# Optimization experiments

Hardware: AMD Instinct MI355X
Metric: run time of the kernel (lower is better)

Reference implementation:

```python
import jax, jax.numpy as jnp
import numpy as np
from jax import lax

B, DIM, H, W = 4, 192, 128, 128
NUM_HEADS = 4
EPS = 1e-12


def _conv1x1(x, w):
    # x: [b,c,h,w], w: [o,i,1,1]
    return lax.conv_general_dilated(x, w, (1, 1), 'VALID',
                                    dimension_numbers=('NCHW', 'OIHW', 'NCHW'))


def _dwconv3x3(x, w):
    # depthwise: w: [c,1,3,3], groups = c
    return lax.conv_general_dilated(x, w, (1, 1), ((1, 1), (1, 1)),
                                    dimension_numbers=('NCHW', 'OIHW', 'NCHW'),
                                    feature_group_count=w.shape[0])


def _l2norm(t):
    # normalize along last (spatial) axis, torch F.normalize semantics
    n = jnp.sqrt(jnp.sum(t * t, axis=-1, keepdims=True))
    return t / jnp.maximum(n, EPS)


def _heads(t, b, h, w):
    # [b, head*c, h, w] -> [b, head, c, h*w]
    return t.reshape(b, NUM_HEADS, t.shape[1] // NUM_HEADS, h * w)


def setup_inputs() -> dict:
    key = jax.random.key(0)
    ks = jax.random.split(key, 9)
    s = 0.02
    return {
        'x': jax.random.normal(ks[0], (B, DIM, H, W), jnp.float32),
        'ctx': jax.random.normal(ks[1], (B, DIM, H, W), jnp.float32),
        'x_qkv_w': jax.random.normal(ks[2], (DIM * 3, DIM, 1, 1), jnp.float32) * s,
        'x_dw_w': jax.random.normal(ks[3], (DIM * 3, 1, 3, 3), jnp.float32) * s,
        'x_po_w': jax.random.normal(ks[4], (DIM, DIM, 1, 1), jnp.float32) * s,
        'ctx_qkv_w': jax.random.normal(ks[5], (DIM * 3, DIM, 1, 1), jnp.float32) * s,
        'ctx_dw_w': jax.random.normal(ks[6], (DIM * 3, 1, 3, 3), jnp.float32) * s,
        'ctx_po_w': jax.random.normal(ks[7], (DIM, DIM, 1, 1), jnp.float32) * s,
        'temperature': jnp.ones((NUM_HEADS, 1, 1), jnp.float32),
    }


def reference(x, ctx, x_qkv_w, x_dw_w, x_po_w, ctx_qkv_w, ctx_dw_w, ctx_po_w, temperature):
    b, c, h, w = x.shape
    x_qkv = _dwconv3x3(_conv1x1(x, x_qkv_w), x_dw_w)
    x_q, x_k, x_v = jnp.split(x_qkv, 3, axis=1)
    ctx_qkv = _dwconv3x3(_conv1x1(ctx, ctx_qkv_w), ctx_dw_w)
    ctx_q, ctx_k, ctx_v = jnp.split(ctx_qkv, 3, axis=1)

    x_q, x_k, x_v = (_heads(t, b, h, w) for t in (x_q, x_k, x_v))
    ctx_q, ctx_k, ctx_v = (_heads(t, b, h, w) for t in (ctx_q, ctx_k, ctx_v))

    temp = temperature[None]  # [1, head, 1, 1]

    # ctx branch: x_q attends over ctx
    q1 = _l2norm(x_q)
    k1 = _l2norm(ctx_k)
    attn1 = jax.nn.softmax(jnp.einsum('bhcn,bhdn->bhcd', q1, k1) * temp, axis=-1)
    ctx_out = jnp.einsum('bhcd,bhdn->bhcn', attn1, ctx_v).reshape(b, c, h, w)
    ctx_out = _conv1x1(ctx_out, ctx_po_w)

    # x branch: ctx_q attends over x
    q2 = _l2norm(ctx_q)
    k2 = _l2norm(x_k)
    attn2 = jax.nn.softmax(jnp.einsum('bhcn,bhdn->bhcd', q2, k2) * temp, axis=-1)
    x_out = jnp.einsum('bhcd,bhdn->bhcn', attn2, x_v).reshape(b, c, h, w)
    x_out = _conv1x1(x_out, x_po_w)

    return (x_out, ctx_out)
```

## Files before the change

### kernel.cpp

```cpp
#include <hip/hip_runtime.h>
#include <hip/hip_bf16.h>

#define N_PIX 16384
#define W_ 128

typedef __attribute__((ext_vector_type(8))) unsigned short ushort8_t;
typedef __attribute__((ext_vector_type(4))) unsigned short ushort4_t;
typedef __attribute__((ext_vector_type(8))) __bf16 bf16x8;
typedef __attribute__((ext_vector_type(4))) float f32x4;

__device__ inline float bf2f(unsigned short u) {
    return __uint_as_float(((unsigned)u) << 16);
}
__device__ inline unsigned short f2bf(float f) {
    __hip_bfloat16 h = __float2bfloat16(f);
    return *(unsigned short*)&h;
}

__global__ __launch_bounds__(256) void k_conv_mfma(
    const float* __restrict__ in,
    const float* __restrict__ w,
    unsigned short* __restrict__ out)
{
    const int p0 = blockIdx.x * 128;
    const int b  = blockIdx.y;
    const float* inb = in + (long)b * 192 * N_PIX;
    unsigned short* ob = out + (long)b * 576 * N_PIX;

    __shared__ unsigned short Xl[128 * 200];
    __shared__ unsigned short Wl[2][96 * 200];

    const int tid  = threadIdx.x;
    const int lane = tid & 63;
    const int wid  = tid >> 6;
    const int wo   = wid >> 1;
    const int wp   = wid & 1;
    const int l15  = lane & 15;
    const int lq   = lane >> 4;

    {
        const int p = tid & 127, kh = tid >> 7;
        #pragma unroll
        for (int seg = 0; seg < 12; seg++) {
            ushort8_t pk;
            #pragma unroll
            for (int j = 0; j < 8; j++)
                pk[j] = f2bf(inb[(long)(kh * 96 + seg * 8 + j) * N_PIX + p0 + p]);
            *(ushort8_t*)&Xl[p * 200 + kh * 96 + seg * 8] = pk;
        }
    }
    #pragma unroll
    for (int it = 0; it < 18; it++) {
        int idx = it * 1024 + tid * 4;
        float4 v = *(const float4*)(w + idx);
        int row = idx / 192, col = idx - row * 192;
        ushort4_t s; s[0] = f2bf(v.x); s[1] = f2bf(v.y); s[2] = f2bf(v.z); s[3] = f2bf(v.w);
        *(ushort4_t*)&Wl[0][row * 200 + col] = s;
    }

    for (int oc = 0; oc < 6; oc++) {
        __syncthreads();
        if (oc + 1 < 6) {
            const float* wc = w + (long)(oc + 1) * 96 * 192;
            #pragma unroll
            for (int it = 0; it < 18; it++) {
                int idx = it * 1024 + tid * 4;
                float4 v = *(const float4*)(wc + idx);
                int row = idx / 192, col = idx - row * 192;
                ushort4_t s; s[0] = f2bf(v.x); s[1] = f2bf(v.y); s[2] = f2bf(v.z); s[3] = f2bf(v.w);
                *(ushort4_t*)&Wl[(oc + 1) & 1][row * 200 + col] = s;
            }
        }
        const unsigned short* Wb = Wl[oc & 1];
        f32x4 acc[3][4];
        const f32x4 zero = {0.f, 0.f, 0.f, 0.f};
        #pragma unroll
        for (int i = 0; i < 3; i++)
            #pragma unroll
            for (int j = 0; j < 4; j++) acc[i][j] = zero;

        #pragma unroll
        for (int kc = 0; kc < 6; kc++) {
            bf16x8 af[3], bfv[4];
            #pragma unroll
            for (int mt = 0; mt < 3; mt++)
                af[mt] = *(const bf16x8*)&Wb[(wo * 48 + mt * 16 + l15) * 200 + kc * 32 + lq * 8];
            #pragma unroll
            for (int nt = 0; nt < 4; nt++)
                bfv[nt] = *(const bf16x8*)&Xl[(wp * 64 + nt * 16 + l15) * 200 + kc * 32 + lq * 8];
            #pragma unroll
            for (int mt = 0; mt < 3; mt++)
                #pragma unroll
                for (int nt = 0; nt < 4; nt++)
                    acc[mt][nt] = __builtin_amdgcn_mfma_f32_16x16x32_bf16(
                        af[mt], bfv[nt], acc[mt][nt], 0, 0, 0);
        }
        #pragma unroll
        for (int mt = 0; mt < 3; mt++) {
            #pragma unroll
            for (int r = 0; r < 4; r++) {
                int o = oc * 96 + wo * 48 + mt * 16 + lq * 4 + r;
                long base = (long)o * N_PIX + p0 + wp * 64 + l15;
                #pragma unroll
                for (int nt = 0; nt < 4; nt++)
                    ob[base + nt * 16] = f2bf(acc[mt][nt][r]);
            }
        }
    }
}

__global__ __launch_bounds__(256) void k_dwconv(
    const unsigned short* __restrict__ in, const float* __restrict__ w,
    unsigned short* __restrict__ out)
{
    const int m  = blockIdx.y;
    const int ch = m % 576;
    const int y0 = blockIdx.x * 16;
    const unsigned short* ip = in + (long)m * N_PIX;
    const float* wp = w + ch * 9;

    __shared__ unsigned short Ll[18][136];

    const int tid = threadIdx.x;
    #pragma unroll
    for (int idx = tid; idx < 288; idx += 256) {
        int lr = idx >> 4, lc = (idx & 15) * 8;
        int gy = y0 - 1 + lr;
        ushort8_t v;
        #pragma unroll
        for (int j = 0; j < 8; j++) v[j] = 0;
        if ((unsigned)gy <= 127u)
            v = *(const ushort8_t*)(ip + gy * W_ + lc);
        *(ushort8_t*)&Ll[lr][lc] = v;
    }
    float wv[9];
    #pragma unroll
    for (int i = 0; i < 9; i++) wv[i] = wp[i];
    __syncthreads();

    const int r  = tid >> 4;
    const int xg = (tid & 15) * 8;

    float o[8];
    #pragma unroll
    for (int j = 0; j < 8; j++) o[j] = 0.f;

    #pragma unroll
    for (int dy = 0; dy < 3; dy++) {
        const unsigned short* lrow = &Ll[r + dy][0];
        float c[10];
        c[0] = (xg == 0) ? 0.f : bf2f(lrow[xg - 1]);
        ushort8_t mid = *(const ushort8_t*)&lrow[xg];
        #pragma unroll
        for (int j = 0; j < 8; j++) c[1 + j] = bf2f(mid[j]);
        c[9] = (xg == 120) ? 0.f : bf2f(lrow[xg + 8]);
        const float w0 = wv[dy * 3], w1 = wv[dy * 3 + 1], w2 = wv[dy * 3 + 2];
        #pragma unroll
        for (int j = 0; j < 8; j++)
            o[j] = fmaf(w0, c[j], fmaf(w1, c[j + 1], fmaf(w2, c[j + 2], o[j])));
    }
    ushort8_t res;
    #pragma unroll
    for (int j = 0; j < 8; j++) res[j] = f2bf(o[j]);
    *(ushort8_t*)(out + (long)m * N_PIX + (y0 + r) * W_ + xg) = res;
}

__global__ __launch_bounds__(256) void k_gram_mfma(
    const unsigned short* __restrict__ qkv_x,
    const unsigned short* __restrict__ qkv_c,
    float* __restrict__ S, float* __restrict__ qn, float* __restrict__ kn)
{
    const int attn = blockIdx.z;
    const int bh   = blockIdx.y;
    const int b = bh >> 2, h = bh & 3;
    const unsigned short* qb =
        (attn == 0 ? qkv_x : qkv_c) + ((long)b * 576 + h * 48) * N_PIX;
    const unsigned short* kb =
        (attn == 0 ? qkv_c : qkv_x) + ((long)b * 576 + 192 + h * 48) * N_PIX;

    __shared__ float Sl[48 * 49];
    __shared__ float qnl[48], knl[48];

    const int tid = threadIdx.x;
    for (int i = tid; i < 48 * 49; i += 256) Sl[i] = 0.f;
    if (tid < 48) { qnl[tid] = 0.f; knl[tid] = 0.f; }
    __syncthreads();

    const int lane = tid & 63, wid = tid >> 6;
    const int l15 = lane & 15, lq = lane >> 4;
    const long nbase = (long)blockIdx.x * 1024 + wid * 256;

    f32x4 acc[3][3], aq[3], ak[3];
    const f32x4 zero = {0.f, 0.f, 0.f, 0.f};
    #pragma unroll
    for (int i = 0; i < 3; i++) {
        aq[i] = zero; ak[i] = zero;
        #pragma unroll
        for (int j = 0; j < 3; j++) acc[i][j] = zero;
    }

    for (int ks = 0; ks < 8; ks++) {
        const long ns = nbase + ks * 32;
        bf16x8 af[3], bfv[3];
        #pragma unroll
        for (int mt = 0; mt < 3; mt++)
            af[mt] = *(const bf16x8*)(qb + (long)(mt * 16 + l15) * N_PIX + ns + lq * 8);
        #pragma unroll
        for (int nt = 0; nt < 3; nt++)
            bfv[nt] = *(const bf16x8*)(kb + (long)(nt * 16 + l15) * N_PIX + ns + lq * 8);
        #pragma unroll
        for (int mt = 0; mt < 3; mt++)
            #pragma unroll
            for (int nt = 0; nt < 3; nt++)
                acc[mt][nt] = __builtin_amdgcn_mfma_f32_16x16x32_bf16(
                    af[mt], bfv[nt], acc[mt][nt], 0, 0, 0);
        #pragma unroll
        for (int mt = 0; mt < 3; mt++)
            aq[mt] = __builtin_amdgcn_mfma_f32_16x16x32_bf16(af[mt], af[mt], aq[mt], 0, 0, 0);
        #pragma unroll
        for (int nt = 0; nt < 3; nt++)
            ak[nt] = __builtin_amdgcn_mfma_f32_16x16x32_bf16(bfv[nt], bfv[nt], ak[nt], 0, 0, 0);
    }

    #pragma unroll
    for (int mt = 0; mt < 3; mt++)
        #pragma unroll
        for (int nt = 0; nt < 3; nt++)
            #pragma unroll
            for (int r = 0; r < 4; r++)
                atomicAdd(&Sl[(mt * 16 + lq * 4 + r) * 49 + nt * 16 + l15],
                          acc[mt][nt][r]);
    #pragma unroll
    for (int mt = 0; mt < 3; mt++)
        #pragma unroll
        for (int r = 0; r < 4; r++)
            if (l15 == lq * 4 + r) {
                atomicAdd(&qnl[mt * 16 + l15], aq[mt][r]);
                atomicAdd(&knl[mt * 16 + l15], ak[mt][r]);
            }
    __syncthreads();

    float* Sg = S + (long)(attn * 16 + bh) * 2304;
    float* qg = qn + (long)(attn * 16 + bh) * 48;
    float* kg = kn + (long)(attn * 16 + bh) * 48;
    for (int i = tid; i < 2304; i += 256) {
        int row = i / 48, col = i - row * 48;
        atomicAdd(&Sg[i], Sl[row * 49 + col]);
    }
    if (tid < 48) atomicAdd(&qg[tid], qnl[tid]);
    else if (tid < 96) atomicAdd(&kg[tid - 48], knl[tid - 48]);
}

__global__ __launch_bounds__(192) void k_softmax(
    const float* __restrict__ S, const float* __restrict__ qn,
    const float* __restrict__ kn, const float* __restrict__ temp,
    float* __restrict__ P)
{
    const int attn = blockIdx.x, b = blockIdx.y;
    const int r = threadIdx.x;
    const int h = r / 48, c = r % 48;
    const int bh = b * 4 + h;
    const float t = temp[h];
    const float* Srow = S + ((long)(attn * 16 + bh) * 48 + c) * 48;
    const float* knp  = kn + (long)(attn * 16 + bh) * 48;
    const float qc = fmaxf(sqrtf(qn[(long)(attn * 16 + bh) * 48 + c]), 1e-12f);
    float lg[48];
    float mx = -1e30f;
    #pragma unroll
    for (int d = 0; d < 48; d++) {
        float kd = fmaxf(sqrtf(knp[d]), 1e-12f);
        lg[d] = Srow[d] / (qc * kd) * t;
        mx = fmaxf(mx, lg[d]);
    }
    float sum = 0.f;
    #pragma unroll
    for (int d = 0; d < 48; d++) { lg[d] = __expf(lg[d] - mx); sum += lg[d]; }
    const float inv = 1.f / sum;
    float* Pp = P + (((long)(attn * 4 + b) * 4 + h) * 48 + c) * 48;
    #pragma unroll
    for (int d = 0; d < 48; d++) Pp[d] = lg[d] * inv;
}

__global__ __launch_bounds__(192) void k_w2(
    const float* __restrict__ P, const float* __restrict__ x_po,
    const float* __restrict__ ctx_po, unsigned short* __restrict__ W2)
{
    const int h = blockIdx.x, b = blockIdx.y, attn = blockIdx.z;
    const float* po = (attn == 0) ? ctx_po : x_po;
    __shared__ float Pl[48][48];
    const float* Pp = P + ((long)(attn * 4 + b) * 4 + h) * 2304;
    for (int it = 0; it < 12; it++) {
        int idx = it * 192 + threadIdx.x;
        Pl[idx / 48][idx % 48] = Pp[idx];
    }
    __syncthreads();
    const int o = threadIdx.x;
    float acc[48];
    #pragma unroll
    for (int d = 0; d < 48; d++) acc[d] = 0.f;
    for (int c = 0; c < 48; c++) {
        float pv = po[(long)o * 192 + h * 48 + c];
        #pragma unroll
        for (int d = 0; d < 48; d++)
            acc[d] = fmaf(pv, Pl[c][d], acc[d]);
    }
    unsigned short* wp = W2 + ((long)(attn * 4 + b) * 192 + o) * 192 + h * 48;
    #pragma unroll
    for (int d = 0; d < 48; d++) wp[d] = f2bf(acc[d]);
}

__global__ __launch_bounds__(256) void k_gemm_v(
    const unsigned short* __restrict__ qkv_x,
    const unsigned short* __restrict__ qkv_c,
    const unsigned short* __restrict__ W2bf,
    float* __restrict__ out)
{
    const int p0 = blockIdx.x * 128;
    const int z  = blockIdx.y;
    const int br = z >> 2, b = z & 3;
    const unsigned short* v =
        (br == 0 ? qkv_x : qkv_c) + (long)b * 576 * N_PIX + 384L * N_PIX;
    const unsigned short* wb =
        W2bf + ((long)((br == 0 ? 1 : 0) * 4 + b)) * 36864;
    float* ob = out + (long)br * 12582912 + (long)b * 192 * N_PIX;

    __shared__ unsigned short Xl[128 * 200];

    const int tid  = threadIdx.x;
    const int lane = tid & 63;
    const int wid  = tid >> 6;
    const int wo   = wid >> 1;
    const int wp   = wid & 1;
    const int l15  = lane & 15;
    const int lq   = lane >> 4;

    {
        const int p = tid & 127, kh = tid >> 7;
        #pragma unroll
        for (int seg = 0; seg < 12; seg++) {
            ushort8_t pk;
            #pragma unroll
            for (int j = 0; j < 8; j++)
                pk[j] = v[(long)(kh * 96 + seg * 8 + j) * N_PIX + p0 + p];
            *(ushort8_t*)&Xl[p * 200 + kh * 96 + seg * 8] = pk;
        }
    }
    __syncthreads();

    #pragma unroll
    for (int oc = 0; oc < 2; oc++) {
        f32x4 acc[3][4];
        const f32x4 zero = {0.f, 0.f, 0.f, 0.f};
        #pragma unroll
        for (int i = 0; i < 3; i++)
            #pragma unroll
            for (int j = 0; j < 4; j++) acc[i][j] = zero;

        #pragma unroll
        for (int kc = 0; kc < 6; kc++) {
            bf16x8 af[3], bfv[4];
            #pragma unroll
            for (int mt = 0; mt < 3; mt++)
                af[mt] = *(const bf16x8*)(wb +
                    (long)(oc * 96 + wo * 48 + mt * 16 + l15) * 192 + kc * 32 + lq * 8);
            #pragma unroll
            for (int nt = 0; nt < 4; nt++)
                bfv[nt] = *(const bf16x8*)&Xl[(wp * 64 + nt * 16 + l15) * 200 + kc * 32 + lq * 8];
            #pragma unroll
            for (int mt = 0; mt < 3; mt++)
                #pragma unroll
                for (int nt = 0; nt < 4; nt++)
                    acc[mt][nt] = __builtin_amdgcn_mfma_f32_16x16x32_bf16(
                        af[mt], bfv[nt], acc[mt][nt], 0, 0, 0);
        }
        #pragma unroll
        for (int mt = 0; mt < 3; mt++) {
            #pragma unroll
            for (int r = 0; r < 4; r++) {
                int o = oc * 96 + wo * 48 + mt * 16 + lq * 4 + r;
                long base = (long)o * N_PIX + p0 + wp * 64 + l15;
                #pragma unroll
                for (int nt = 0; nt < 4; nt++)
                    ob[base + nt * 16] = acc[mt][nt][r];
            }
        }
    }
}

extern "C" void kernel_launch(void* const* d_in, const int* in_sizes, int n_in,
                              void* d_out, int out_size, void* d_ws, size_t ws_size,
                              hipStream_t stream) {
    (void)in_sizes; (void)n_in; (void)out_size; (void)ws_size;
    const float* x       = (const float*)d_in[0];
    const float* ctx     = (const float*)d_in[1];
    const float* x_qkv_w = (const float*)d_in[2];
    const float* x_dw_w  = (const float*)d_in[3];
    const float* x_po_w  = (const float*)d_in[4];
    const float* c_qkv_w = (const float*)d_in[5];
    const float* c_dw_w  = (const float*)d_in[6];
    const float* c_po_w  = (const float*)d_in[7];
    const float* temp    = (const float*)d_in[8];
    float* out = (float*)d_out;

    const long QKV = 37748736L;
    unsigned short* qkv_x16 = (unsigned short*)d_ws;
    unsigned short* qkv_c16 = qkv_x16 + QKV;
    float* S  = (float*)(qkv_c16 + QKV);
    float* qn = S + 73728;
    float* kn = qn + 1536;
    float* P  = kn + 1536;
    unsigned short* W2bf = (unsigned short*)(P + 73728);

    hipMemsetAsync(S, 0, (73728 + 1536 + 1536) * sizeof(float), stream);

    unsigned short* tmp16 = (unsigned short*)d_out;

    k_conv_mfma<<<dim3(128, 4), 256, 0, stream>>>(x, x_qkv_w, tmp16);
    k_dwconv<<<dim3(8, 2304), 256, 0, stream>>>(tmp16, x_dw_w, qkv_x16);
    k_conv_mfma<<<dim3(128, 4), 256, 0, stream>>>(ctx, c_qkv_w, tmp16);
    k_dwconv<<<dim3(8, 2304), 256, 0, stream>>>(tmp16, c_dw_w, qkv_c16);

    k_gram_mfma<<<dim3(16, 16, 2), 256, 0, stream>>>(qkv_x16, qkv_c16, S, qn, kn);
    k_softmax<<<dim3(2, 4), dim3(192), 0, stream>>>(S, qn, kn, temp, P);
    k_w2<<<dim3(4, 4, 2), dim3(192), 0, stream>>>(P, x_po_w, c_po_w, W2bf);

    k_gemm_v<<<dim3(128, 8), 256, 0, stream>>>(qkv_x16, qkv_c16, W2bf, out);
}
```

Before: 424.1 us.

## Prepack qkv weights to bf16, halve pixel tiles, read weights from global

Adds a small kernel that converts the 1x1 qkv weights to bf16 once, so the conv kernel reads A-fragments straight from global or L2 and no longer stages weights through double-buffered LDS. Both the conv and final V-GEMM kernels now use 64-pixel tiles with each of four waves owning 48 output rows. This halves LDS use, doubles grid size, and adds launch bounds that target three blocks per CU. The cost is more global weight reads per block, reloading each activation tile in more blocks, and two extra small launches.

```diff
diff --git a/kernel.cpp b/kernel.cpp
--- a/kernel.cpp
+++ b/kernel.cpp
@@ -17,61 +17,49 @@
     return *(unsigned short*)&h;
 }
 
-__global__ __launch_bounds__(256) void k_conv_mfma(
+__global__ __launch_bounds__(256) void k_pack_w(
+    const float* __restrict__ w, unsigned short* __restrict__ o)
+{
+    const int i = (blockIdx.x * 256 + threadIdx.x) * 4;
+    float4 v = *(const float4*)(w + i);
+    ushort4_t s;
+    s[0] = f2bf(v.x); s[1] = f2bf(v.y); s[2] = f2bf(v.z); s[3] = f2bf(v.w);
+    *(ushort4_t*)(o + i) = s;
+}
+
+__global__ __launch_bounds__(256, 3) void k_conv_mfma(
     const float* __restrict__ in,
-    const float* __restrict__ w,
+    const unsigned short* __restrict__ wbf,
     unsigned short* __restrict__ out)
 {
-    const int p0 = blockIdx.x * 128;
+    const int p0 = blockIdx.x * 64;
     const int b  = blockIdx.y;
     const float* inb = in + (long)b * 192 * N_PIX;
     unsigned short* ob = out + (long)b * 576 * N_PIX;
 
-    __shared__ unsigned short Xl[128 * 200];
-    __shared__ unsigned short Wl[2][96 * 200];
+    __shared__ unsigned short Xl[64 * 200];
 
     const int tid  = threadIdx.x;
     const int lane = tid & 63;
     const int wid  = tid >> 6;
-    const int wo   = wid >> 1;
-    const int wp   = wid & 1;
     const int l15  = lane & 15;
     const int lq   = lane >> 4;
 
     {
-        const int p = tid & 127, kh = tid >> 7;
-        #pragma unroll
-        for (int seg = 0; seg < 12; seg++) {
+        const int p = tid & 63, kg = tid >> 6;
+        #pragma unroll
+        for (int seg = 0; seg < 6; seg++) {
             ushort8_t pk;
             #pragma unroll
             for (int j = 0; j < 8; j++)
-                pk[j] = f2bf(inb[(long)(kh * 96 + seg * 8 + j) * N_PIX + p0 + p]);
-            *(ushort8_t*)&Xl[p * 200 + kh * 96 + seg * 8] = pk;
+                pk[j] = f2bf(inb[(long)(kg * 48 + seg * 8 + j) * N_PIX + p0 + p]);
+            *(ushort8_t*)&Xl[p * 200 + kg * 48 + seg * 8] = pk;
         }
     }
-    #pragma unroll
-    for (int it = 0; it < 18; it++) {
-        int idx = it * 1024 + tid * 4;
-        float4 v = *(const float4*)(w + idx);
-        int row = idx / 192, col = idx - row * 192;
-        ushort4_t s; s[0] = f2bf(v.x); s[1] = f2bf(v.y); s[2] = f2bf(v.z); s[3] = f2bf(v.w);
-        *(ushort4_t*)&Wl[0][row * 200 + col] = s;
-    }
-
-    for (int oc = 0; oc < 6; oc++) {
-        __syncthreads();
-        if (oc + 1 < 6) {
-            const float* wc = w + (long)(oc + 1) * 96 * 192;
-            #pragma unroll
-            for (int it = 0; it < 18; it++) {
-                int idx = it * 1024 + tid * 4;
-                float4 v = *(const float4*)(wc + idx);
-                int row = idx / 192, col = idx - row * 192;
-                ushort4_t s; s[0] = f2bf(v.x); s[1] = f2bf(v.y); s[2] = f2bf(v.z); s[3] = f2bf(v.w);
-                *(ushort4_t*)&Wl[(oc + 1) & 1][row * 200 + col] = s;
-            }
-        }
-        const unsigned short* Wb = Wl[oc & 1];
+    __syncthreads();
+
+    #pragma unroll 1
+    for (int oc = 0; oc < 3; oc++) {
         f32x4 acc[3][4];
         const f32x4 zero = {0.f, 0.f, 0.f, 0.f};
         #pragma unroll
@@ -84,10 +72,11 @@
             bf16x8 af[3], bfv[4];
             #pragma unroll
             for (int mt = 0; mt < 3; mt++)
-                af[mt] = *(const bf16x8*)&Wb[(wo * 48 + mt * 16 + l15) * 200 + kc * 32 + lq * 8];
+                af[mt] = *(const bf16x8*)(wbf +
+                    (long)(oc * 192 + wid * 48 + mt * 16 + l15) * 192 + kc * 32 + lq * 8);
             #pragma unroll
             for (int nt = 0; nt < 4; nt++)
-                bfv[nt] = *(const bf16x8*)&Xl[(wp * 64 + nt * 16 + l15) * 200 + kc * 32 + lq * 8];
+                bfv[nt] = *(const bf16x8*)&Xl[(nt * 16 + l15) * 200 + kc * 32 + lq * 8];
             #pragma unroll
             for (int mt = 0; mt < 3; mt++)
                 #pragma unroll
@@ -99,8 +88,8 @@
         for (int mt = 0; mt < 3; mt++) {
             #pragma unroll
             for (int r = 0; r < 4; r++) {
-                int o = oc * 96 + wo * 48 + mt * 16 + lq * 4 + r;
-                long base = (long)o * N_PIX + p0 + wp * 64 + l15;
+                int o = oc * 192 + wid * 48 + mt * 16 + lq * 4 + r;
+                long base = (long)o * N_PIX + p0 + l15;
                 #pragma unroll
                 for (int nt = 0; nt < 4; nt++)
                     ob[base + nt * 16] = f2bf(acc[mt][nt][r]);
@@ -309,13 +298,13 @@
     for (int d = 0; d < 48; d++) wp[d] = f2bf(acc[d]);
 }
 
-__global__ __launch_bounds__(256) void k_gemm_v(
+__global__ __launch_bounds__(256, 3) void k_gemm_v(
     const unsigned short* __restrict__ qkv_x,
     const unsigned short* __restrict__ qkv_c,
     const unsigned short* __restrict__ W2bf,
     float* __restrict__ out)
 {
-    const int p0 = blockIdx.x * 128;
+    const int p0 = blockIdx.x * 64;
     const int z  = blockIdx.y;
     const int br = z >> 2, b = z & 3;
     const unsigned short* v =
@@ -324,65 +313,60 @@
         W2bf + ((long)((br == 0 ? 1 : 0) * 4 + b)) * 36864;
     float* ob = out + (long)br * 12582912 + (long)b * 192 * N_PIX;
 
-    __shared__ unsigned short Xl[128 * 200];
+    __shared__ unsigned short Xl[64 * 200];
 
     const int tid  = threadIdx.x;
     const int lane = tid & 63;
     const int wid  = tid >> 6;
-    const int wo   = wid >> 1;
-    const int wp   = wid & 1;
     const int l15  = lane & 15;
     const int lq   = lane >> 4;
 
     {
-        const int p = tid & 127, kh = tid >> 7;
-        #pragma unroll
-        for (int seg = 0; seg < 12; seg++) {
+        const int p = tid & 63, kg = tid >> 6;
+        #pragma unroll
+        for (int seg = 0; seg < 6; seg++) {
             ushort8_t pk;
             #pragma unroll
             for (int j = 0; j < 8; j++)
-                pk[j] = v[(long)(kh * 96 + seg * 8 + j) * N_PIX + p0 + p];
-            *(ushort8_t*)&Xl[p * 200 + kh * 96 + seg * 8] = pk;
+                pk[j] = v[(long)(kg * 48 + seg * 8 + j) * N_PIX + p0 + p];
+            *(ushort8_t*)&Xl[p * 200 + kg * 48 + seg * 8] = pk;
         }
     }
     __syncthreads();
 
-    #pragma unroll
-    for (int oc = 0; oc < 2; oc++) {
-        f32x4 acc[3][4];
-        const f32x4 zero = {0.f, 0.f, 0.f, 0.f};
-        #pragma unroll
-        for (int i = 0; i < 3; i++)
-            #pragma unroll
-            for (int j = 0; j < 4; j++) acc[i][j] = zero;
-
-        #pragma unroll
-        for (int kc = 0; kc < 6; kc++) {
-            bf16x8 af[3], bfv[4];
-            #pragma unroll
-            for (int mt = 0; mt < 3; mt++)
-                af[mt] = *(const bf16x8*)(wb +
-                    (long)(oc * 96 + wo * 48 + mt * 16 + l15) * 192 + kc * 32 + lq * 8);
+    f32x4 acc[3][4];
+    const f32x4 zero = {0.f, 0.f, 0.f, 0.f};
+    #pragma unroll
+    for (int i = 0; i < 3; i++)
+        #pragma unroll
+        for (int j = 0; j < 4; j++) acc[i][j] = zero;
+
+    #pragma unroll
+    for (int kc = 0; kc < 6; kc++) {
+        bf16x8 af[3], bfv[4];
+        #pragma unroll
+        for (int mt = 0; mt < 3; mt++)
+            af[mt] = *(const bf16x8*)(wb +
+                (long)(wid * 48 + mt * 16 + l15) * 192 + kc * 32 + lq * 8);
+        #pragma unroll
+        for (int nt = 0; nt < 4; nt++)
+            bfv[nt] = *(const bf16x8*)&Xl[(nt * 16 + l15) * 200 + kc * 32 + lq * 8];
+        #pragma unroll
+        for (int mt = 0; mt < 3; mt++)
             #pragma unroll
             for (int nt = 0; nt < 4; nt++)
-                bfv[nt] = *(const bf16x8*)&Xl[(wp * 64 + nt * 16 + l15) * 200 + kc * 32 + lq * 8];
-            #pragma unroll
-            for (int mt = 0; mt < 3; mt++)
-                #pragma unroll
-                for (int nt = 0; nt < 4; nt++)
-                    acc[mt][nt] = __builtin_amdgcn_mfma_f32_16x16x32_bf16(
-                        af[mt], bfv[nt], acc[mt][nt], 0, 0, 0);
-        }
-        #pragma unroll
-        for (int mt = 0; mt < 3; mt++) {
-            #pragma unroll
-            for (int r = 0; r < 4; r++) {
-                int o = oc * 96 + wo * 48 + mt * 16 + lq * 4 + r;
-                long base = (long)o * N_PIX + p0 + wp * 64 + l15;
-                #pragma unroll
-                for (int nt = 0; nt < 4; nt++)
-                    ob[base + nt * 16] = acc[mt][nt][r];
-            }
+                acc[mt][nt] = __builtin_amdgcn_mfma_f32_16x16x32_bf16(
+                    af[mt], bfv[nt], acc[mt][nt], 0, 0, 0);
+    }
+    #pragma unroll
+    for (int mt = 0; mt < 3; mt++) {
+        #pragma unroll
+        for (int r = 0; r < 4; r++) {
+            int o = wid * 48 + mt * 16 + lq * 4 + r;
+            long base = (long)o * N_PIX + p0 + l15;
+            #pragma unroll
+            for (int nt = 0; nt < 4; nt++)
+                ob[base + nt * 16] = acc[mt][nt][r];
         }
     }
 }
@@ -414,15 +398,20 @@
     hipMemsetAsync(S, 0, (73728 + 1536 + 1536) * sizeof(float), stream);
 
     unsigned short* tmp16 = (unsigned short*)d_out;
-
-    k_conv_mfma<<<dim3(128, 4), 256, 0, stream>>>(x, x_qkv_w, tmp16);
+    unsigned short* wx16  = (unsigned short*)d_out + QKV;
+    unsigned short* wc16  = wx16 + 110592;
+
+    k_pack_w<<<dim3(108), 256, 0, stream>>>(x_qkv_w, wx16);
+    k_pack_w<<<dim3(108), 256, 0, stream>>>(c_qkv_w, wc16);
+
+    k_conv_mfma<<<dim3(256, 4), 256, 0, stream>>>(x, wx16, tmp16);
     k_dwconv<<<dim3(8, 2304), 256, 0, stream>>>(tmp16, x_dw_w, qkv_x16);
-    k_conv_mfma<<<dim3(128, 4), 256, 0, stream>>>(ctx, c_qkv_w, tmp16);
+    k_conv_mfma<<<dim3(256, 4), 256, 0, stream>>>(ctx, wc16, tmp16);
     k_dwconv<<<dim3(8, 2304), 256, 0, stream>>>(tmp16, c_dw_w, qkv_c16);
 
     k_gram_mfma<<<dim3(16, 16, 2), 256, 0, stream>>>(qkv_x16, qkv_c16, S, qn, kn);
     k_softmax<<<dim3(2, 4), dim3(192), 0, stream>>>(S, qn, kn, temp, P);
     k_w2<<<dim3(4, 4, 2), dim3(192), 0, stream>>>(P, x_po_w, c_po_w, W2bf);
 
-    k_gemm_v<<<dim3(128, 8), 256, 0, stream>>>(qkv_x16, qkv_c16, W2bf, out);
-}
+    k_gemm_v<<<dim3(256, 8), 256, 0, stream>>>(qkv_x16, qkv_c16, W2bf, out);
+}
```

Result: slower. 444.0 us (+4.7%).

## Prepack swizzled bf16 conv weights and stream them to LDS asynchronously

Applied to the files above, without the earlier changes.

Adds a small kernel that converts the 1x1 qkv conv weights to bf16 once, in an XOR-swizzled row layout. The conv kernel then copies weight chunks straight into LDS with global_load_lds, replacing per-block float loads, conversion and padded stores. LDS reads use the XOR swizzle instead of padding to avoid bank conflicts, and the barrier moves to the end of each chunk loop. This halves the weight bytes each block fetches and removes redundant per-block conversion, at the cost of two extra tiny launches and scratch space borrowed from the output buffer.

```diff
diff --git a/kernel.cpp b/kernel.cpp
--- a/kernel.cpp
+++ b/kernel.cpp
@@ -17,9 +17,28 @@
     return *(unsigned short*)&h;
 }
 
+__device__ inline void glds16(const unsigned short* g, unsigned short* l) {
+    __builtin_amdgcn_global_load_lds(
+        (const __attribute__((address_space(1))) unsigned int*)g,
+        (__attribute__((address_space(3))) unsigned int*)l, 16, 0, 0);
+}
+
+__global__ __launch_bounds__(256) void k_pack_w_swz(
+    const float* __restrict__ w, unsigned short* __restrict__ o)
+{
+    const int idx = blockIdx.x * 256 + threadIdx.x;
+    const int row = idx / 24, c = idx % 24;
+    const int sc = c ^ (row & 7);
+    const float* src = w + (long)row * 192 + c * 8;
+    ushort8_t s;
+    #pragma unroll
+    for (int j = 0; j < 8; j++) s[j] = f2bf(src[j]);
+    *(ushort8_t*)(o + (long)row * 192 + sc * 8) = s;
+}
+
 __global__ __launch_bounds__(256) void k_conv_mfma(
     const float* __restrict__ in,
-    const float* __restrict__ w,
+    const unsigned short* __restrict__ wswz,
     unsigned short* __restrict__ out)
 {
     const int p0 = blockIdx.x * 128;
@@ -28,7 +47,7 @@
     unsigned short* ob = out + (long)b * 576 * N_PIX;
 
     __shared__ unsigned short Xl[128 * 200];
-    __shared__ unsigned short Wl[2][96 * 200];
+    __shared__ unsigned short Wl[2][96 * 192];
 
     const int tid  = threadIdx.x;
     const int lane = tid & 63;
@@ -39,6 +58,15 @@
     const int lq   = lane >> 4;
 
     {
+        const long cb = (long)wid * 9216;
+        #pragma unroll
+        for (int it = 0; it < 9; it++) {
+            glds16(wswz + (cb + it * 1024) / 2 + lane * 8,
+                   &Wl[0][(cb + it * 1024) / 2]);
+        }
+    }
+
+    {
         const int p = tid & 127, kh = tid >> 7;
         #pragma unroll
         for (int seg = 0; seg < 12; seg++) {
@@ -49,27 +77,16 @@
             *(ushort8_t*)&Xl[p * 200 + kh * 96 + seg * 8] = pk;
         }
     }
-    #pragma unroll
-    for (int it = 0; it < 18; it++) {
-        int idx = it * 1024 + tid * 4;
-        float4 v = *(const float4*)(w + idx);
-        int row = idx / 192, col = idx - row * 192;
-        ushort4_t s; s[0] = f2bf(v.x); s[1] = f2bf(v.y); s[2] = f2bf(v.z); s[3] = f2bf(v.w);
-        *(ushort4_t*)&Wl[0][row * 200 + col] = s;
-    }
-
+    __syncthreads();
+
+    #pragma unroll 1
     for (int oc = 0; oc < 6; oc++) {
-        __syncthreads();
         if (oc + 1 < 6) {
-            const float* wc = w + (long)(oc + 1) * 96 * 192;
-            #pragma unroll
-            for (int it = 0; it < 18; it++) {
-                int idx = it * 1024 + tid * 4;
-                float4 v = *(const float4*)(wc + idx);
-                int row = idx / 192, col = idx - row * 192;
-                ushort4_t s; s[0] = f2bf(v.x); s[1] = f2bf(v.y); s[2] = f2bf(v.z); s[3] = f2bf(v.w);
-                *(ushort4_t*)&Wl[(oc + 1) & 1][row * 200 + col] = s;
-            }
+            const long gb = (long)(oc + 1) * 36864 + (long)wid * 9216;
+            unsigned short* lb = &Wl[(oc + 1) & 1][wid * 4608];
+            #pragma unroll
+            for (int it = 0; it < 9; it++)
+                glds16(wswz + (gb + it * 1024) / 2 + lane * 8, lb + it * 512);
         }
         const unsigned short* Wb = Wl[oc & 1];
         f32x4 acc[3][4];
@@ -83,8 +100,11 @@
         for (int kc = 0; kc < 6; kc++) {
             bf16x8 af[3], bfv[4];
             #pragma unroll
-            for (int mt = 0; mt < 3; mt++)
-                af[mt] = *(const bf16x8*)&Wb[(wo * 48 + mt * 16 + l15) * 200 + kc * 32 + lq * 8];
+            for (int mt = 0; mt < 3; mt++) {
+                const int row = wo * 48 + mt * 16 + l15;
+                const int sc  = (kc * 4 + lq) ^ (l15 & 7);
+                af[mt] = *(const bf16x8*)&Wb[row * 192 + sc * 8];
+            }
             #pragma unroll
             for (int nt = 0; nt < 4; nt++)
                 bfv[nt] = *(const bf16x8*)&Xl[(wp * 64 + nt * 16 + l15) * 200 + kc * 32 + lq * 8];
@@ -106,6 +126,7 @@
                     ob[base + nt * 16] = f2bf(acc[mt][nt][r]);
             }
         }
+        __syncthreads();
     }
 }
 
@@ -414,10 +435,15 @@
     hipMemsetAsync(S, 0, (73728 + 1536 + 1536) * sizeof(float), stream);
 
     unsigned short* tmp16 = (unsigned short*)d_out;
-
-    k_conv_mfma<<<dim3(128, 4), 256, 0, stream>>>(x, x_qkv_w, tmp16);
+    unsigned short* wx16  = (unsigned short*)d_out + QKV;
+    unsigned short* wc16  = wx16 + 110592;
+
+    k_pack_w_swz<<<dim3(54), 256, 0, stream>>>(x_qkv_w, wx16);
+    k_pack_w_swz<<<dim3(54), 256, 0, stream>>>(c_qkv_w, wc16);
+
+    k_conv_mfma<<<dim3(128, 4), 256, 0, stream>>>(x, wx16, tmp16);
     k_dwconv<<<dim3(8, 2304), 256, 0, stream>>>(tmp16, x_dw_w, qkv_x16);
-    k_conv_mfma<<<dim3(128, 4), 256, 0, stream>>>(ctx, c_qkv_w, tmp16);
+    k_conv_mfma<<<dim3(128, 4), 256, 0, stream>>>(ctx, c_qkv_w != 0 ? wc16 : wc16, tmp16);
     k_dwconv<<<dim3(8, 2304), 256, 0, stream>>>(tmp16, c_dw_w, qkv_c16);
 
     k_gram_mfma<<<dim3(16, 16, 2), 256, 0, stream>>>(qkv_x16, qkv_c16, S, qn, kn);
```

Result: faster. 398.3 us (-6.1%).

## Prepack qkv weights to bf16, batch x/ctx conv launches, register-resident weight fragments

Applied to the files above, without the earlier changes.

A small kernel now converts both 1x1 qkv weight matrices to bf16 once. The conv kernel then loads its weight fragments straight from global memory into registers per output chunk, instead of staging fp32-to-bf16 converted copies through double-buffered LDS. When the workspace is large enough, the x and ctx conv and depthwise passes each run as one merged launch, doubling the grid. The second intermediate buffer reuses the S workspace region. The same register preloading and a 2-blocks-per-CU launch bound are applied to k_gemm_v. This trades LDS capacity and barriers for more register pressure and uncached-looking global weight reads, and it depends on the workspace size at runtime.

```diff
diff --git a/kernel.cpp b/kernel.cpp
--- a/kernel.cpp
+++ b/kernel.cpp
@@ -17,18 +17,34 @@
     return *(unsigned short*)&h;
 }
 
-__global__ __launch_bounds__(256) void k_conv_mfma(
-    const float* __restrict__ in,
-    const float* __restrict__ w,
-    unsigned short* __restrict__ out)
+__global__ __launch_bounds__(256) void k_pack_w(
+    const float* __restrict__ wa, const float* __restrict__ wb,
+    unsigned short* __restrict__ oa, unsigned short* __restrict__ ob)
+{
+    const int blk = blockIdx.x;
+    const float* w = (blk < 108) ? wa : wb;
+    unsigned short* o = (blk < 108) ? oa : ob;
+    const int i = ((blk % 108) * 256 + threadIdx.x) * 4;
+    float4 v = *(const float4*)(w + i);
+    ushort4_t s;
+    s[0] = f2bf(v.x); s[1] = f2bf(v.y); s[2] = f2bf(v.z); s[3] = f2bf(v.w);
+    *(ushort4_t*)(o + i) = s;
+}
+
+__global__ __launch_bounds__(256, 2) void k_conv_mfma(
+    const float* __restrict__ x, const float* __restrict__ ctx,
+    const unsigned short* __restrict__ wx, const unsigned short* __restrict__ wc,
+    unsigned short* __restrict__ ox, unsigned short* __restrict__ octx)
 {
     const int p0 = blockIdx.x * 128;
-    const int b  = blockIdx.y;
-    const float* inb = in + (long)b * 192 * N_PIX;
-    unsigned short* ob = out + (long)b * 576 * N_PIX;
+    const int bb = blockIdx.y;
+    const int b  = bb & 3;
+    const bool isx = bb < 4;
+    const float* inb = (isx ? x : ctx) + (long)b * 192 * N_PIX;
+    const unsigned short* wbf = isx ? wx : wc;
+    unsigned short* ob = (isx ? ox : octx) + (long)b * 576 * N_PIX;
 
     __shared__ unsigned short Xl[128 * 200];
-    __shared__ unsigned short Wl[2][96 * 200];
 
     const int tid  = threadIdx.x;
     const int lane = tid & 63;
@@ -49,29 +65,18 @@
             *(ushort8_t*)&Xl[p * 200 + kh * 96 + seg * 8] = pk;
         }
     }
-    #pragma unroll
-    for (int it = 0; it < 18; it++) {
-        int idx = it * 1024 + tid * 4;
-        float4 v = *(const float4*)(w + idx);
-        int row = idx / 192, col = idx - row * 192;
-        ushort4_t s; s[0] = f2bf(v.x); s[1] = f2bf(v.y); s[2] = f2bf(v.z); s[3] = f2bf(v.w);
-        *(ushort4_t*)&Wl[0][row * 200 + col] = s;
-    }
-
+    __syncthreads();
+
+    #pragma unroll 1
     for (int oc = 0; oc < 6; oc++) {
-        __syncthreads();
-        if (oc + 1 < 6) {
-            const float* wc = w + (long)(oc + 1) * 96 * 192;
-            #pragma unroll
-            for (int it = 0; it < 18; it++) {
-                int idx = it * 1024 + tid * 4;
-                float4 v = *(const float4*)(wc + idx);
-                int row = idx / 192, col = idx - row * 192;
-                ushort4_t s; s[0] = f2bf(v.x); s[1] = f2bf(v.y); s[2] = f2bf(v.z); s[3] = f2bf(v.w);
-                *(ushort4_t*)&Wl[(oc + 1) & 1][row * 200 + col] = s;
-            }
-        }
-        const unsigned short* Wb = Wl[oc & 1];
+        bf16x8 af[3][6];
+        #pragma unroll
+        for (int mt = 0; mt < 3; mt++)
+            #pragma unroll
+            for (int kc = 0; kc < 6; kc++)
+                af[mt][kc] = *(const bf16x8*)(wbf +
+                    (long)(oc * 96 + wo * 48 + mt * 16 + l15) * 192 + kc * 32 + lq * 8);
+
         f32x4 acc[3][4];
         const f32x4 zero = {0.f, 0.f, 0.f, 0.f};
         #pragma unroll
@@ -81,10 +86,7 @@
 
         #pragma unroll
         for (int kc = 0; kc < 6; kc++) {
-            bf16x8 af[3], bfv[4];
-            #pragma unroll
-            for (int mt = 0; mt < 3; mt++)
-                af[mt] = *(const bf16x8*)&Wb[(wo * 48 + mt * 16 + l15) * 200 + kc * 32 + lq * 8];
+            bf16x8 bfv[4];
             #pragma unroll
             for (int nt = 0; nt < 4; nt++)
                 bfv[nt] = *(const bf16x8*)&Xl[(wp * 64 + nt * 16 + l15) * 200 + kc * 32 + lq * 8];
@@ -93,7 +95,7 @@
                 #pragma unroll
                 for (int nt = 0; nt < 4; nt++)
                     acc[mt][nt] = __builtin_amdgcn_mfma_f32_16x16x32_bf16(
-                        af[mt], bfv[nt], acc[mt][nt], 0, 0, 0);
+                        af[mt][kc], bfv[nt], acc[mt][nt], 0, 0, 0);
         }
         #pragma unroll
         for (int mt = 0; mt < 3; mt++) {
@@ -110,14 +112,18 @@
 }
 
 __global__ __launch_bounds__(256) void k_dwconv(
-    const unsigned short* __restrict__ in, const float* __restrict__ w,
-    unsigned short* __restrict__ out)
-{
-    const int m  = blockIdx.y;
+    const unsigned short* __restrict__ tx, const unsigned short* __restrict__ tc,
+    const float* __restrict__ wxd, const float* __restrict__ wcd,
+    unsigned short* __restrict__ qx, unsigned short* __restrict__ qc)
+{
+    const int mz = blockIdx.y;
+    const int br = (mz >= 2304) ? 1 : 0;
+    const int m  = mz - br * 2304;
     const int ch = m % 576;
     const int y0 = blockIdx.x * 16;
-    const unsigned short* ip = in + (long)m * N_PIX;
-    const float* wp = w + ch * 9;
+    const unsigned short* ip = (br ? tc : tx) + (long)m * N_PIX;
+    const float* wp = (br ? wcd : wxd) + ch * 9;
+    unsigned short* op = (br ? qc : qx) + (long)m * N_PIX;
 
     __shared__ unsigned short Ll[18][136];
 
@@ -162,7 +168,7 @@
     ushort8_t res;
     #pragma unroll
     for (int j = 0; j < 8; j++) res[j] = f2bf(o[j]);
-    *(ushort8_t*)(out + (long)m * N_PIX + (y0 + r) * W_ + xg) = res;
+    *(ushort8_t*)(op + (y0 + r) * W_ + xg) = res;
 }
 
 __global__ __launch_bounds__(256) void k_gram_mfma(
@@ -309,7 +315,7 @@
     for (int d = 0; d < 48; d++) wp[d] = f2bf(acc[d]);
 }
 
-__global__ __launch_bounds__(256) void k_gemm_v(
+__global__ __launch_bounds__(256, 2) void k_gemm_v(
     const unsigned short* __restrict__ qkv_x,
     const unsigned short* __restrict__ qkv_c,
     const unsigned short* __restrict__ W2bf,
@@ -347,8 +353,16 @@
     }
     __syncthreads();
 
-    #pragma unroll
+    #pragma unroll 1
     for (int oc = 0; oc < 2; oc++) {
+        bf16x8 af[3][6];
+        #pragma unroll
+        for (int mt = 0; mt < 3; mt++)
+            #pragma unroll
+            for (int kc = 0; kc < 6; kc++)
+                af[mt][kc] = *(const bf16x8*)(wb +
+                    (long)(oc * 96 + wo * 48 + mt * 16 + l15) * 192 + kc * 32 + lq * 8);
+
         f32x4 acc[3][4];
         const f32x4 zero = {0.f, 0.f, 0.f, 0.f};
         #pragma unroll
@@ -358,11 +372,7 @@
 
         #pragma unroll
         for (int kc = 0; kc < 6; kc++) {
-            bf16x8 af[3], bfv[4];
-            #pragma unroll
-            for (int mt = 0; mt < 3; mt++)
-                af[mt] = *(const bf16x8*)(wb +
-                    (long)(oc * 96 + wo * 48 + mt * 16 + l15) * 192 + kc * 32 + lq * 8);
+            bf16x8 bfv[4];
             #pragma unroll
             for (int nt = 0; nt < 4; nt++)
                 bfv[nt] = *(const bf16x8*)&Xl[(wp * 64 + nt * 16 + l15) * 200 + kc * 32 + lq * 8];
@@ -371,7 +381,7 @@
                 #pragma unroll
                 for (int nt = 0; nt < 4; nt++)
                     acc[mt][nt] = __builtin_amdgcn_mfma_f32_16x16x32_bf16(
-                        af[mt], bfv[nt], acc[mt][nt], 0, 0, 0);
+                        af[mt][kc], bfv[nt], acc[mt][nt], 0, 0, 0);
         }
         #pragma unroll
         for (int mt = 0; mt < 3; mt++) {
@@ -390,7 +400,7 @@
 extern "C" void kernel_launch(void* const* d_in, const int* in_sizes, int n_in,
                               void* d_out, int out_size, void* d_ws, size_t ws_size,
                               hipStream_t stream) {
-    (void)in_sizes; (void)n_in; (void)out_size; (void)ws_size;
+    (void)in_sizes; (void)n_in; (void)out_size;
     const float* x       = (const float*)d_in[0];
     const float* ctx     = (const float*)d_in[1];
     const float* x_qkv_w = (const float*)d_in[2];
@@ -411,14 +421,31 @@
     float* P  = kn + 1536;
     unsigned short* W2bf = (unsigned short*)(P + 73728);
 
+    unsigned short* tmp_x = (unsigned short*)d_out;
+    unsigned short* wx16  = (unsigned short*)d_out + QKV;
+    unsigned short* wc16  = wx16 + 110592;
+
+    k_pack_w<<<dim3(216), 256, 0, stream>>>(x_qkv_w, c_qkv_w, wx16, wc16);
+
+    const size_t ws_needed = (size_t)QKV * 2 * 3;
+    if (ws_size >= ws_needed) {
+        unsigned short* tmp_c = (unsigned short*)S;
+        k_conv_mfma<<<dim3(128, 8), 256, 0, stream>>>(
+            x, ctx, wx16, wc16, tmp_x, tmp_c);
+        k_dwconv<<<dim3(8, 4608), 256, 0, stream>>>(
+            tmp_x, tmp_c, x_dw_w, c_dw_w, qkv_x16, qkv_c16);
+    } else {
+        k_conv_mfma<<<dim3(128, 4), 256, 0, stream>>>(
+            x, x, wx16, wx16, tmp_x, tmp_x);
+        k_dwconv<<<dim3(8, 2304), 256, 0, stream>>>(
+            tmp_x, tmp_x, x_dw_w, x_dw_w, qkv_x16, qkv_x16);
+        k_conv_mfma<<<dim3(128, 4), 256, 0, stream>>>(
+            ctx, ctx, wc16, wc16, tmp_x, tmp_x);
+        k_dwconv<<<dim3(8, 2304), 256, 0, stream>>>(
+            tmp_x, tmp_x, c_dw_w, c_dw_w, qkv_c16, qkv_c16);
+    }
+
     hipMemsetAsync(S, 0, (73728 + 1536 + 1536) * sizeof(float), stream);
-
-    unsigned short* tmp16 = (unsigned short*)d_out;
-
-    k_conv_mfma<<<dim3(128, 4), 256, 0, stream>>>(x, x_qkv_w, tmp16);
-    k_dwconv<<<dim3(8, 2304), 256, 0, stream>>>(tmp16, x_dw_w, qkv_x16);
-    k_conv_mfma<<<dim3(128, 4), 256, 0, stream>>>(ctx, c_qkv_w, tmp16);
-    k_dwconv<<<dim3(8, 2304), 256, 0, stream>>>(tmp16, c_dw_w, qkv_c16);
 
     k_gram_mfma<<<dim3(16, 16, 2), 256, 0, stream>>>(qkv_x16, qkv_c16, S, qn, kn);
     k_softmax<<<dim3(2, 4), dim3(192), 0, stream>>>(S, qn, kn, temp, P);
```

New measurement: 410.0 us. 1.03x faster.
